# Performance work log

Hardware: AMD Instinct MI355X
Metric: run time of the kernel (lower is better)

The kernel has to match this reference:

```python
import jax, jax.numpy as jnp
import numpy as np


def setup_inputs() -> dict:
    key = jax.random.key(0)
    embeddings = jax.random.normal(key, (4, 2048, 128), dtype=jnp.float32)
    return {"embeddings": embeddings}


def _pairwise_dist(x):
    # x: [N, D] -> Euclidean distance matrix [N, N] (matches torch.cdist, p=2)
    sq = jnp.sum(x * x, axis=-1)  # [N]
    d2 = sq[:, None] + sq[None, :] - 2.0 * (x @ x.T)
    d2 = jnp.maximum(d2, 0.0)
    # safe sqrt: exact 0 on the diagonal / coincident points, no NaN grads
    safe = jnp.where(d2 > 0.0, d2, 1.0)
    return jnp.where(d2 > 0.0, jnp.sqrt(safe), 0.0)


def reference(embeddings) -> jnp.ndarray:
    b, s, d = embeddings.shape
    x = embeddings.reshape(b * s, d)
    dist = _pairwise_dist(x)                 # [N, N]
    mean_dist = jnp.mean(dist)
    # torch.std default: unbiased (ddof=1) over all elements
    std_dist = jnp.std(dist, ddof=1)
    return std_dist / (mean_dist + 1e-08)
```

## Files before the change

kernel.cpp:

```cpp
#include <hip/hip_runtime.h>
#include <hip/hip_bf16.h>
#include <math.h>


#define NPTS   8192
#define DIM    128
#define TILE   128
#define KHALF  64
#define NTILES (NPTS / TILE)
#define NTOT   (NTILES * (NTILES + 1) / 2)

typedef __attribute__((ext_vector_type(8))) short short8;
typedef __attribute__((ext_vector_type(4))) float f32x4;

typedef const __attribute__((address_space(1))) void* gas_ptr;
typedef __attribute__((address_space(3))) void* las_ptr;

__device__ __forceinline__ void gload16(const void* g, void* l) {
    __builtin_amdgcn_global_load_lds((gas_ptr)g, (las_ptr)l, 16, 0, 0);
}

__global__ __launch_bounds__(256)
void ph_prep(const float* __restrict__ x, ushort* __restrict__ xb,
             float* __restrict__ sq)
{
    const int tid = threadIdx.x;
    const int row = blockIdx.x * 32 + (tid >> 3);
    const int seg = tid & 7;
    const float4* p = reinterpret_cast<const float4*>(x + (size_t)row * DIM + seg * 16);
    float v[16];
    {
        float4 a = p[0], b = p[1], c = p[2], d = p[3];
        v[0]=a.x; v[1]=a.y; v[2]=a.z; v[3]=a.w;  v[4]=b.x; v[5]=b.y; v[6]=b.z; v[7]=b.w;
        v[8]=c.x; v[9]=c.y; v[10]=c.z; v[11]=c.w; v[12]=d.x; v[13]=d.y; v[14]=d.z; v[15]=d.w;
    }
    float s = 0.f;
    ushort h[16];
#pragma unroll
    for (int j = 0; j < 16; ++j) {
        __hip_bfloat16 hb = __float2bfloat16(v[j]);
        h[j] = *reinterpret_cast<ushort*>(&hb);
        s = fmaf(v[j], v[j], s);
    }
    short8 o0, o1;
#pragma unroll
    for (int j = 0; j < 8; ++j) { o0[j] = (short)h[j]; o1[j] = (short)h[j+8]; }
    short8* dst = reinterpret_cast<short8*>(xb + (size_t)row * DIM + seg * 16);
    dst[0] = o0; dst[1] = o1;
    s += __shfl_xor(s, 1); s += __shfl_xor(s, 2); s += __shfl_xor(s, 4);
    if (seg == 0) sq[row] = s;
}

__global__ __launch_bounds__(256)
void ph_gram(const ushort* __restrict__ xb, const float* __restrict__ sq,
             double* __restrict__ partials)
{
    const int f   = blockIdx.x;
    const int tid = threadIdx.x;

    int bi = (int)((129.0f - sqrtf((float)(16641 - 8 * f))) * 0.5f);
    while ((bi + 1) * 64 - ((bi + 1) * bi) / 2 <= f) ++bi;
    while (bi * 64 - (bi * (bi - 1)) / 2 > f) --bi;
    const int bj = bi + (f - (bi * 64 - (bi * (bi - 1)) / 2));

    __shared__ ushort As[TILE * KHALF];
    __shared__ ushort Bs[TILE * KHALF];
    __shared__ float  nA[TILE], nB[TILE];
    __shared__ double rr[8];

    const int lane = tid & 63;
    const int wv   = tid >> 6;
    const int wr   = wv >> 1, wc = wv & 1;

    if (tid < 128) nA[tid]       = sq[bi * TILE + tid];
    else           nB[tid - 128] = sq[bj * TILE + (tid - 128)];

    const char* gA = (const char*)(xb + (size_t)bi * TILE * DIM);
    const char* gB = (const char*)(xb + (size_t)bj * TILE * DIM);

    const int srow = lane >> 3;
    const int skb  = (lane & 7) * 16;
#define STAGE(h)                                                              \
    {                                                                         \
        _Pragma("unroll")                                                     \
        for (int c = 0; c < 4; ++c) {                                         \
            const int chunk = wv * 4 + c;                                     \
            const int row   = chunk * 8 + srow;                               \
            const int gkb   = (h) * 128 + (skb ^ ((row & 7) << 4));           \
            const size_t go = (size_t)row * 256 + gkb;                        \
            gload16(gA + go, (char*)As + chunk * 1024);                       \
            gload16(gB + go, (char*)Bs + chunk * 1024);                       \
        }                                                                     \
    }

    f32x4 acc[4][4];
#pragma unroll
    for (int m = 0; m < 4; ++m)
#pragma unroll
        for (int n = 0; n < 4; ++n) acc[m][n] = (f32x4){0.f, 0.f, 0.f, 0.f};

    STAGE(0);
    __syncthreads();

#pragma unroll
    for (int h = 0; h < 2; ++h) {
#pragma unroll
        for (int kk = 0; kk < 2; ++kk) {
            const int kb = kk * 64 + (lane >> 4) * 16;
            short8 af[4], bfr[4];
#pragma unroll
            for (int m = 0; m < 4; ++m) {
                const int row = wr * 64 + m * 16 + (lane & 15);
                af[m] = *reinterpret_cast<const short8*>(
                    (const char*)As + row * 128 + (kb ^ ((row & 7) << 4)));
            }
#pragma unroll
            for (int n = 0; n < 4; ++n) {
                const int col = wc * 64 + n * 16 + (lane & 15);
                bfr[n] = *reinterpret_cast<const short8*>(
                    (const char*)Bs + col * 128 + (kb ^ ((col & 7) << 4)));
            }
#pragma unroll
            for (int m = 0; m < 4; ++m)
#pragma unroll
                for (int n = 0; n < 4; ++n)
                    acc[m][n] = __builtin_amdgcn_mfma_f32_16x16x32_bf16(
                        af[m], bfr[n], acc[m][n], 0, 0, 0);
        }
        if (h == 0) {
            __syncthreads();
            STAGE(1);
            __syncthreads();
        }
    }

    float s1 = 0.f, s2 = 0.f;
    const bool diag = (bi == bj);
#pragma unroll
    for (int m = 0; m < 4; ++m) {
        float nAr[4];
#pragma unroll
        for (int r = 0; r < 4; ++r) nAr[r] = nA[wr*64 + m*16 + (lane>>4)*4 + r];
#pragma unroll
        for (int n = 0; n < 4; ++n) {
            const int col  = wc*64 + n*16 + (lane & 15);
            const float nBc = nB[col];
#pragma unroll
            for (int r = 0; r < 4; ++r) {
                float d2 = fmaf(-2.f, acc[m][n][r], nAr[r] + nBc);
                d2 = fmaxf(d2, 0.f);
                if (diag) {
                    const int row = wr*64 + m*16 + (lane>>4)*4 + r;
                    if (row == col) d2 = 0.f;
                }
                s1 += sqrtf(d2);
                s2 += d2;
            }
        }
    }
#pragma unroll
    for (int off = 1; off < 64; off <<= 1) {
        s1 += __shfl_xor(s1, off);
        s2 += __shfl_xor(s2, off);
    }
    const double w = diag ? 1.0 : 2.0;
    if (lane == 0) { rr[wv] = (double)s1 * w; rr[4 + wv] = (double)s2 * w; }
    __syncthreads();
    if (tid == 0) {
        partials[2*f]     = rr[0] + rr[1] + rr[2] + rr[3];
        partials[2*f + 1] = rr[4] + rr[5] + rr[6] + rr[7];
    }
#undef STAGE
}

__global__ __launch_bounds__(256)
void ph_finalize(const double* __restrict__ partials, float* __restrict__ out)
{
    __shared__ double r1[256], r2[256];
    const int tid = threadIdx.x;
    double s1 = 0.0, s2 = 0.0;
    for (int i = tid; i < NTOT; i += 256) { s1 += partials[2*i]; s2 += partials[2*i+1]; }
    r1[tid] = s1; r2[tid] = s2;
    __syncthreads();
    for (int off = 128; off > 0; off >>= 1) {
        if (tid < off) { r1[tid] += r1[tid+off]; r2[tid] += r2[tid+off]; }
        __syncthreads();
    }
    if (tid == 0) {
        const double M    = (double)NPTS * (double)NPTS;
        const double mean = r1[0] / M;
        double var = (r2[0] - r1[0]*r1[0]/M) / (M - 1.0);
        if (var < 0.0) var = 0.0;
        out[0] = (float)(sqrt(var) / (mean + 1e-8));
    }
}

#define LSTR 132
__global__ __launch_bounds__(256)
void ph_pair_kernel(const float* __restrict__ x, double* __restrict__ partials)
{
    const int bi  = blockIdx.y;
    const int bj  = blockIdx.x;
    const int tid = threadIdx.x;
    const int flat = bi * NTILES + bj;
    if (bj < bi) {
        if (tid == 0) { partials[2*flat] = 0.0; partials[2*flat+1] = 0.0; }
        return;
    }
    __shared__ __align__(16) float As[TILE * LSTR];
    __shared__ __align__(16) float Bs[TILE * LSTR];
    __shared__ float  nA[TILE];
    __shared__ float  nB[TILE];
    __shared__ double red1[256];
    __shared__ double red2[256];
    const float* Ab = x + (size_t)bi * TILE * DIM;
    const float* Bb = x + (size_t)bj * TILE * DIM;
#pragma unroll
    for (int it = 0; it < 16; ++it) {
        const int e   = (tid + it * 256) * 4;
        const int row = e >> 7;
        const int k   = e & 127;
        float4 va = *reinterpret_cast<const float4*>(Ab + e);
        As[(k+0)*LSTR + row] = va.x; As[(k+1)*LSTR + row] = va.y;
        As[(k+2)*LSTR + row] = va.z; As[(k+3)*LSTR + row] = va.w;
        float4 vb = *reinterpret_cast<const float4*>(Bb + e);
        Bs[(k+0)*LSTR + row] = vb.x; Bs[(k+1)*LSTR + row] = vb.y;
        Bs[(k+2)*LSTR + row] = vb.z; Bs[(k+3)*LSTR + row] = vb.w;
    }
    __syncthreads();
    if (tid < 128) {
        float s = 0.f;
#pragma unroll 8
        for (int k = 0; k < DIM; ++k) { float v = As[k*LSTR + tid]; s = fmaf(v, v, s); }
        nA[tid] = s;
    } else {
        const int r = tid - 128;
        float s = 0.f;
#pragma unroll 8
        for (int k = 0; k < DIM; ++k) { float v = Bs[k*LSTR + r]; s = fmaf(v, v, s); }
        nB[r] = s;
    }
    __syncthreads();
    const int tx = tid & 15, ty = tid >> 4;
    const int ra = ty * 8, cb = tx * 8;
    float acc[8][8];
#pragma unroll
    for (int r = 0; r < 8; ++r)
#pragma unroll
        for (int c = 0; c < 8; ++c) acc[r][c] = 0.f;
#pragma unroll 4
    for (int k = 0; k < DIM; ++k) {
        const float4 a0 = *reinterpret_cast<const float4*>(&As[k*LSTR + ra]);
        const float4 a1 = *reinterpret_cast<const float4*>(&As[k*LSTR + ra + 4]);
        const float4 b0 = *reinterpret_cast<const float4*>(&Bs[k*LSTR + cb]);
        const float4 b1 = *reinterpret_cast<const float4*>(&Bs[k*LSTR + cb + 4]);
        const float a[8] = {a0.x,a0.y,a0.z,a0.w,a1.x,a1.y,a1.z,a1.w};
        const float b[8] = {b0.x,b0.y,b0.z,b0.w,b1.x,b1.y,b1.z,b1.w};
#pragma unroll
        for (int r = 0; r < 8; ++r)
#pragma unroll
            for (int c = 0; c < 8; ++c)
                acc[r][c] = fmaf(a[r], b[c], acc[r][c]);
    }
    double s1 = 0.0, s2 = 0.0;
    const int gi0 = bi*TILE + ra, gj0 = bj*TILE + cb;
#pragma unroll
    for (int r = 0; r < 8; ++r) {
#pragma unroll
        for (int c = 0; c < 8; ++c) {
            float d2 = nA[ra+r] + nB[cb+c] - 2.0f * acc[r][c];
            d2 = fmaxf(d2, 0.0f);
            if (gi0 + r == gj0 + c) d2 = 0.0f;
            s1 += (double)sqrtf(d2);
            s2 += (double)d2;
        }
    }
    const double w = (bi == bj) ? 1.0 : 2.0;
    s1 *= w; s2 *= w;
    red1[tid] = s1; red2[tid] = s2;
    __syncthreads();
    for (int off = 128; off > 0; off >>= 1) {
        if (tid < off) { red1[tid] += red1[tid+off]; red2[tid] += red2[tid+off]; }
        __syncthreads();
    }
    if (tid == 0) { partials[2*flat] = red1[0]; partials[2*flat+1] = red2[0]; }
}

__global__ __launch_bounds__(256)
void ph_finalize_sq(const double* __restrict__ partials, float* __restrict__ out)
{
    __shared__ double r1[256], r2[256];
    const int tid = threadIdx.x;
    double s1 = 0.0, s2 = 0.0;
    for (int i = tid; i < NTILES*NTILES; i += 256) { s1 += partials[2*i]; s2 += partials[2*i+1]; }
    r1[tid] = s1; r2[tid] = s2;
    __syncthreads();
    for (int off = 128; off > 0; off >>= 1) {
        if (tid < off) { r1[tid] += r1[tid+off]; r2[tid] += r2[tid+off]; }
        __syncthreads();
    }
    if (tid == 0) {
        const double M    = (double)NPTS * (double)NPTS;
        const double mean = r1[0] / M;
        double var = (r2[0] - r1[0]*r1[0]/M) / (M - 1.0);
        if (var < 0.0) var = 0.0;
        out[0] = (float)(sqrt(var) / (mean + 1e-8));
    }
}

extern "C" void kernel_launch(void* const* d_in, const int* in_sizes, int n_in,
                              void* d_out, int out_size, void* d_ws, size_t ws_size,
                              hipStream_t stream)
{
    const float* x = (const float*)d_in[0];
    float* out     = (float*)d_out;

    const size_t XB_OFF = 0;
    const size_t SQ_OFF = (size_t)NPTS * DIM * sizeof(ushort);
    const size_t PT_OFF = SQ_OFF + NPTS * sizeof(float);
    const size_t NEEDED = PT_OFF + (size_t)NTOT * 2 * sizeof(double);

    if (ws_size >= NEEDED) {
        ushort* xb       = (ushort*)((char*)d_ws + XB_OFF);
        float*  sq       = (float*) ((char*)d_ws + SQ_OFF);
        double* partials = (double*)((char*)d_ws + PT_OFF);

        ph_prep<<<NPTS / 32, 256, 0, stream>>>(x, xb, sq);
        ph_gram<<<NTOT, 256, 0, stream>>>(xb, sq, partials);
        ph_finalize<<<1, 256, 0, stream>>>(partials, out);
    } else {
        double* partials = (double*)d_ws;
        ph_pair_kernel<<<dim3(NTILES, NTILES), 256, 0, stream>>>(x, partials);
        ph_finalize_sq<<<1, 256, 0, stream>>>(partials, out);
    }
}
```

Measured before the change: 41.82 us.

## Load MFMA operands directly from global memory, dropping LDS staging

The gram kernel no longer stages A/B tiles through LDS with global_load_lds and barriers. Each lane now loads its bf16 MFMA fragments straight from global (L2-resident) memory, and reads the squared norms from global too. Launch bounds now request 3 blocks per CU. This removes the LDS traffic and the mid-loop syncs, but each wave reloads data its neighbours share, which raises global/L2 traffic and exposes load latency.

```diff
diff --git a/kernel.cpp b/kernel.cpp
--- a/kernel.cpp
+++ b/kernel.cpp
@@ -6,19 +6,11 @@
 #define NPTS   8192
 #define DIM    128
 #define TILE   128
-#define KHALF  64
 #define NTILES (NPTS / TILE)
 #define NTOT   (NTILES * (NTILES + 1) / 2)
 
 typedef __attribute__((ext_vector_type(8))) short short8;
 typedef __attribute__((ext_vector_type(4))) float f32x4;
-
-typedef const __attribute__((address_space(1))) void* gas_ptr;
-typedef __attribute__((address_space(3))) void* las_ptr;
-
-__device__ __forceinline__ void gload16(const void* g, void* l) {
-    __builtin_amdgcn_global_load_lds((gas_ptr)g, (las_ptr)l, 16, 0, 0);
-}
 
 __global__ __launch_bounds__(256)
 void ph_prep(const float* __restrict__ x, ushort* __restrict__ xb,
@@ -51,7 +43,7 @@
     if (seg == 0) sq[row] = s;
 }
 
-__global__ __launch_bounds__(256)
+__global__ __launch_bounds__(256, 3)
 void ph_gram(const ushort* __restrict__ xb, const float* __restrict__ sq,
              double* __restrict__ partials)
 {
@@ -63,35 +55,20 @@
     while (bi * 64 - (bi * (bi - 1)) / 2 > f) --bi;
     const int bj = bi + (f - (bi * 64 - (bi * (bi - 1)) / 2));
 
-    __shared__ ushort As[TILE * KHALF];
-    __shared__ ushort Bs[TILE * KHALF];
-    __shared__ float  nA[TILE], nB[TILE];
-    __shared__ double rr[8];
-
     const int lane = tid & 63;
     const int wv   = tid >> 6;
     const int wr   = wv >> 1, wc = wv & 1;
 
-    if (tid < 128) nA[tid]       = sq[bi * TILE + tid];
-    else           nB[tid - 128] = sq[bj * TILE + (tid - 128)];
-
-    const char* gA = (const char*)(xb + (size_t)bi * TILE * DIM);
-    const char* gB = (const char*)(xb + (size_t)bj * TILE * DIM);
-
-    const int srow = lane >> 3;
-    const int skb  = (lane & 7) * 16;
-#define STAGE(h)                                                              \
-    {                                                                         \
-        _Pragma("unroll")                                                     \
-        for (int c = 0; c < 4; ++c) {                                         \
-            const int chunk = wv * 4 + c;                                     \
-            const int row   = chunk * 8 + srow;                               \
-            const int gkb   = (h) * 128 + (skb ^ ((row & 7) << 4));           \
-            const size_t go = (size_t)row * 256 + gkb;                        \
-            gload16(gA + go, (char*)As + chunk * 1024);                       \
-            gload16(gB + go, (char*)Bs + chunk * 1024);                       \
-        }                                                                     \
-    }
+    const char* base = (const char*)xb;
+    const int   koff = (lane >> 4) * 16;
+    const char* pA[4];
+    const char* pB[4];
+#pragma unroll
+    for (int m = 0; m < 4; ++m)
+        pA[m] = base + (size_t)(bi*TILE + wr*64 + m*16 + (lane & 15)) * 256 + koff;
+#pragma unroll
+    for (int n = 0; n < 4; ++n)
+        pB[n] = base + (size_t)(bj*TILE + wc*64 + n*16 + (lane & 15)) * 256 + koff;
 
     f32x4 acc[4][4];
 #pragma unroll
@@ -99,52 +76,36 @@
 #pragma unroll
         for (int n = 0; n < 4; ++n) acc[m][n] = (f32x4){0.f, 0.f, 0.f, 0.f};
 
-    STAGE(0);
-    __syncthreads();
-
-#pragma unroll
-    for (int h = 0; h < 2; ++h) {
-#pragma unroll
-        for (int kk = 0; kk < 2; ++kk) {
-            const int kb = kk * 64 + (lane >> 4) * 16;
-            short8 af[4], bfr[4];
-#pragma unroll
-            for (int m = 0; m < 4; ++m) {
-                const int row = wr * 64 + m * 16 + (lane & 15);
-                af[m] = *reinterpret_cast<const short8*>(
-                    (const char*)As + row * 128 + (kb ^ ((row & 7) << 4)));
-            }
-#pragma unroll
-            for (int n = 0; n < 4; ++n) {
-                const int col = wc * 64 + n * 16 + (lane & 15);
-                bfr[n] = *reinterpret_cast<const short8*>(
-                    (const char*)Bs + col * 128 + (kb ^ ((col & 7) << 4)));
-            }
-#pragma unroll
-            for (int m = 0; m < 4; ++m)
-#pragma unroll
-                for (int n = 0; n < 4; ++n)
-                    acc[m][n] = __builtin_amdgcn_mfma_f32_16x16x32_bf16(
-                        af[m], bfr[n], acc[m][n], 0, 0, 0);
-        }
-        if (h == 0) {
-            __syncthreads();
-            STAGE(1);
-            __syncthreads();
-        }
-    }
-
+#pragma unroll
+    for (int kk = 0; kk < 4; ++kk) {
+        short8 af[4], bfr[4];
+#pragma unroll
+        for (int m = 0; m < 4; ++m)
+            af[m]  = *reinterpret_cast<const short8*>(pA[m] + kk * 64);
+#pragma unroll
+        for (int n = 0; n < 4; ++n)
+            bfr[n] = *reinterpret_cast<const short8*>(pB[n] + kk * 64);
+#pragma unroll
+        for (int m = 0; m < 4; ++m)
+#pragma unroll
+            for (int n = 0; n < 4; ++n)
+                acc[m][n] = __builtin_amdgcn_mfma_f32_16x16x32_bf16(
+                    af[m], bfr[n], acc[m][n], 0, 0, 0);
+    }
+
+    const float* sqA = sq + bi * TILE;
+    const float* sqB = sq + bj * TILE;
     float s1 = 0.f, s2 = 0.f;
     const bool diag = (bi == bj);
 #pragma unroll
     for (int m = 0; m < 4; ++m) {
         float nAr[4];
 #pragma unroll
-        for (int r = 0; r < 4; ++r) nAr[r] = nA[wr*64 + m*16 + (lane>>4)*4 + r];
+        for (int r = 0; r < 4; ++r) nAr[r] = sqA[wr*64 + m*16 + (lane>>4)*4 + r];
 #pragma unroll
         for (int n = 0; n < 4; ++n) {
-            const int col  = wc*64 + n*16 + (lane & 15);
-            const float nBc = nB[col];
+            const int col   = wc*64 + n*16 + (lane & 15);
+            const float nBc = sqB[col];
 #pragma unroll
             for (int r = 0; r < 4; ++r) {
                 float d2 = fmaf(-2.f, acc[m][n][r], nAr[r] + nBc);
@@ -163,6 +124,8 @@
         s1 += __shfl_xor(s1, off);
         s2 += __shfl_xor(s2, off);
     }
+
+    __shared__ double rr[8];
     const double w = diag ? 1.0 : 2.0;
     if (lane == 0) { rr[wv] = (double)s1 * w; rr[4 + wv] = (double)s2 * w; }
     __syncthreads();
@@ -170,7 +133,6 @@
         partials[2*f]     = rr[0] + rr[1] + rr[2] + rr[3];
         partials[2*f + 1] = rr[4] + rr[5] + rr[6] + rr[7];
     }
-#undef STAGE
 }
 
 __global__ __launch_bounds__(256)
```

Result: slower. 59.74 us (+42.9%).

## Load full K tiles into LDS in one stage and read norms from registers

Applied to the files above, without the earlier changes.

The Gram kernel now stages the whole 128-wide K dimension of both tiles into shared memory in one pass, instead of two halves separated by barriers. Removing the mid-loop sync-restage-sync sequence lets all global loads be in flight together. The squared norms are loaded straight from global memory into registers rather than going through shared memory. The epilogue is split into diagonal and off-diagonal paths with two accumulators each for more ILP. Shared memory per block doubles to 64 KB, which may limit how many blocks fit on each CU.

```diff
diff --git a/kernel.cpp b/kernel.cpp
--- a/kernel.cpp
+++ b/kernel.cpp
@@ -6,7 +6,6 @@
 #define NPTS   8192
 #define DIM    128
 #define TILE   128
-#define KHALF  64
 #define NTILES (NPTS / TILE)
 #define NTOT   (NTILES * (NTILES + 1) / 2)
 
@@ -63,35 +62,37 @@
     while (bi * 64 - (bi * (bi - 1)) / 2 > f) --bi;
     const int bj = bi + (f - (bi * 64 - (bi * (bi - 1)) / 2));
 
-    __shared__ ushort As[TILE * KHALF];
-    __shared__ ushort Bs[TILE * KHALF];
-    __shared__ float  nA[TILE], nB[TILE];
+    __shared__ ushort As[TILE * DIM];
+    __shared__ ushort Bs[TILE * DIM];
     __shared__ double rr[8];
 
     const int lane = tid & 63;
     const int wv   = tid >> 6;
     const int wr   = wv >> 1, wc = wv & 1;
 
-    if (tid < 128) nA[tid]       = sq[bi * TILE + tid];
-    else           nB[tid - 128] = sq[bj * TILE + (tid - 128)];
-
     const char* gA = (const char*)(xb + (size_t)bi * TILE * DIM);
     const char* gB = (const char*)(xb + (size_t)bj * TILE * DIM);
 
-    const int srow = lane >> 3;
-    const int skb  = (lane & 7) * 16;
-#define STAGE(h)                                                              \
-    {                                                                         \
-        _Pragma("unroll")                                                     \
-        for (int c = 0; c < 4; ++c) {                                         \
-            const int chunk = wv * 4 + c;                                     \
-            const int row   = chunk * 8 + srow;                               \
-            const int gkb   = (h) * 128 + (skb ^ ((row & 7) << 4));           \
-            const size_t go = (size_t)row * 256 + gkb;                        \
-            gload16(gA + go, (char*)As + chunk * 1024);                       \
-            gload16(gB + go, (char*)Bs + chunk * 1024);                       \
-        }                                                                     \
-    }
+    const int srow = lane >> 4;
+    const int skb  = (lane & 15) * 16;
+#pragma unroll
+    for (int c = 0; c < 8; ++c) {
+        const int chunk = wv * 8 + c;
+        const int row   = chunk * 4 + srow;
+        const int kbl   = skb ^ ((row & 7) << 4);
+        const size_t go = (size_t)row * 256 + kbl;
+        gload16(gA + go, (char*)As + chunk * 1024);
+        gload16(gB + go, (char*)Bs + chunk * 1024);
+    }
+
+    const float* sqA = sq + bi * TILE + wr * 64 + (lane >> 4) * 4;
+    const float* sqB = sq + bj * TILE + wc * 64 + (lane & 15);
+    float4 nAr[4];
+    float  nBc[4];
+#pragma unroll
+    for (int m = 0; m < 4; ++m) nAr[m] = *reinterpret_cast<const float4*>(sqA + m * 16);
+#pragma unroll
+    for (int n = 0; n < 4; ++n) nBc[n] = sqB[n * 16];
 
     f32x4 acc[4][4];
 #pragma unroll
@@ -99,65 +100,71 @@
 #pragma unroll
         for (int n = 0; n < 4; ++n) acc[m][n] = (f32x4){0.f, 0.f, 0.f, 0.f};
 
-    STAGE(0);
-    __syncthreads();
-
-#pragma unroll
-    for (int h = 0; h < 2; ++h) {
-#pragma unroll
-        for (int kk = 0; kk < 2; ++kk) {
-            const int kb = kk * 64 + (lane >> 4) * 16;
-            short8 af[4], bfr[4];
-#pragma unroll
-            for (int m = 0; m < 4; ++m) {
-                const int row = wr * 64 + m * 16 + (lane & 15);
-                af[m] = *reinterpret_cast<const short8*>(
-                    (const char*)As + row * 128 + (kb ^ ((row & 7) << 4)));
+    __syncthreads();
+
+#pragma unroll
+    for (int kk = 0; kk < 4; ++kk) {
+        const int kb = kk * 64 + (lane >> 4) * 16;
+        short8 af[4], bfr[4];
+#pragma unroll
+        for (int m = 0; m < 4; ++m) {
+            const int row = wr * 64 + m * 16 + (lane & 15);
+            af[m] = *reinterpret_cast<const short8*>(
+                (const char*)As + row * 256 + (kb ^ ((row & 7) << 4)));
+        }
+#pragma unroll
+        for (int n = 0; n < 4; ++n) {
+            const int col = wc * 64 + n * 16 + (lane & 15);
+            bfr[n] = *reinterpret_cast<const short8*>(
+                (const char*)Bs + col * 256 + (kb ^ ((col & 7) << 4)));
+        }
+#pragma unroll
+        for (int m = 0; m < 4; ++m)
+#pragma unroll
+            for (int n = 0; n < 4; ++n)
+                acc[m][n] = __builtin_amdgcn_mfma_f32_16x16x32_bf16(
+                    af[m], bfr[n], acc[m][n], 0, 0, 0);
+    }
+
+    float s1a = 0.f, s1b = 0.f, s2a = 0.f, s2b = 0.f;
+    const bool diag = (bi == bj);
+    if (!diag) {
+#pragma unroll
+        for (int m = 0; m < 4; ++m) {
+#pragma unroll
+            for (int n = 0; n < 4; ++n) {
+                const float pre0 = nAr[m].x + nBc[n];
+                const float pre1 = nAr[m].y + nBc[n];
+                const float pre2 = nAr[m].z + nBc[n];
+                const float pre3 = nAr[m].w + nBc[n];
+                float d0 = fmaxf(fmaf(-2.f, acc[m][n][0], pre0), 0.f);
+                float d1 = fmaxf(fmaf(-2.f, acc[m][n][1], pre1), 0.f);
+                float d2 = fmaxf(fmaf(-2.f, acc[m][n][2], pre2), 0.f);
+                float d3 = fmaxf(fmaf(-2.f, acc[m][n][3], pre3), 0.f);
+                s1a += sqrtf(d0); s1b += sqrtf(d1);
+                s1a += sqrtf(d2); s1b += sqrtf(d3);
+                s2a += d0 + d2;   s2b += d1 + d3;
             }
+        }
+    } else {
+#pragma unroll
+        for (int m = 0; m < 4; ++m) {
 #pragma unroll
             for (int n = 0; n < 4; ++n) {
-                const int col = wc * 64 + n * 16 + (lane & 15);
-                bfr[n] = *reinterpret_cast<const short8*>(
-                    (const char*)Bs + col * 128 + (kb ^ ((col & 7) << 4)));
+#pragma unroll
+                for (int r = 0; r < 4; ++r) {
+                    const int row = wr*64 + m*16 + (lane>>4)*4 + r;
+                    const int col = wc*64 + n*16 + (lane & 15);
+                    const float nA_ = (r==0)?nAr[m].x:(r==1)?nAr[m].y:(r==2)?nAr[m].z:nAr[m].w;
+                    float d2 = fmaxf(fmaf(-2.f, acc[m][n][r], nA_ + nBc[n]), 0.f);
+                    if (row == col) d2 = 0.f;
+                    s1a += sqrtf(d2);
+                    s2a += d2;
+                }
             }
-#pragma unroll
-            for (int m = 0; m < 4; ++m)
-#pragma unroll
-                for (int n = 0; n < 4; ++n)
-                    acc[m][n] = __builtin_amdgcn_mfma_f32_16x16x32_bf16(
-                        af[m], bfr[n], acc[m][n], 0, 0, 0);
-        }
-        if (h == 0) {
-            __syncthreads();
-            STAGE(1);
-            __syncthreads();
-        }
-    }
-
-    float s1 = 0.f, s2 = 0.f;
-    const bool diag = (bi == bj);
-#pragma unroll
-    for (int m = 0; m < 4; ++m) {
-        float nAr[4];
-#pragma unroll
-        for (int r = 0; r < 4; ++r) nAr[r] = nA[wr*64 + m*16 + (lane>>4)*4 + r];
-#pragma unroll
-        for (int n = 0; n < 4; ++n) {
-            const int col  = wc*64 + n*16 + (lane & 15);
-            const float nBc = nB[col];
-#pragma unroll
-            for (int r = 0; r < 4; ++r) {
-                float d2 = fmaf(-2.f, acc[m][n][r], nAr[r] + nBc);
-                d2 = fmaxf(d2, 0.f);
-                if (diag) {
-                    const int row = wr*64 + m*16 + (lane>>4)*4 + r;
-                    if (row == col) d2 = 0.f;
-                }
-                s1 += sqrtf(d2);
-                s2 += d2;
-            }
-        }
-    }
+        }
+    }
+    float s1 = (s1a + s1b), s2 = (s2a + s2b);
 #pragma unroll
     for (int off = 1; off < 64; off <<= 1) {
         s1 += __shfl_xor(s1, off);
@@ -170,7 +177,6 @@
         partials[2*f]     = rr[0] + rr[1] + rr[2] + rr[3];
         partials[2*f + 1] = rr[4] + rr[5] + rr[6] + rr[7];
     }
-#undef STAGE
 }
 
 __global__ __launch_bounds__(256)
```

After: 44.11 us. +5.5%, slower.

## Enlarge gram tiles to 256x256 with 512 threads and double-buffered K staging

Applied to the files above, without the earlier changes.

The gram kernel now processes 256x256 output tiles with 8 waves, each holding an 8x4 MFMA accumulator block. The two K halves are staged into separate LDS buffers, so the second half's load overlaps the first half's compute and one barrier is dropped. The epilogue reads norms directly from global memory, uses a hardware sqrt builtin, and splits accumulators to break dependency chains. The changes aim to raise reuse and cut per-block overhead, but there are now only 528 blocks on a 256-CU part, which increases tail imbalance, and LDS and register use per block go up.

```diff
diff --git a/kernel.cpp b/kernel.cpp
--- a/kernel.cpp
+++ b/kernel.cpp
@@ -5,10 +5,11 @@
 
 #define NPTS   8192
 #define DIM    128
-#define TILE   128
-#define KHALF  64
-#define NTILES (NPTS / TILE)
-#define NTOT   (NTILES * (NTILES + 1) / 2)
+#define BT     256
+#define NT2    (NPTS / BT)
+#define NBLK   (NT2 * (NT2 + 1) / 2)
+#define NTILES (NPTS / 128)
+#define NTOTSQ (NTILES * NTILES)
 
 typedef __attribute__((ext_vector_type(8))) short short8;
 typedef __attribute__((ext_vector_type(4))) float f32x4;
@@ -18,6 +19,10 @@
 
 __device__ __forceinline__ void gload16(const void* g, void* l) {
     __builtin_amdgcn_global_load_lds((gas_ptr)g, (las_ptr)l, 16, 0, 0);
+}
+
+__device__ __forceinline__ float fsqrt(float x) {
+    return __builtin_amdgcn_sqrtf(x);
 }
 
 __global__ __launch_bounds__(256)
@@ -51,126 +56,148 @@
     if (seg == 0) sq[row] = s;
 }
 
-__global__ __launch_bounds__(256)
+__global__ __launch_bounds__(512)
 void ph_gram(const ushort* __restrict__ xb, const float* __restrict__ sq,
              double* __restrict__ partials)
 {
     const int f   = blockIdx.x;
     const int tid = threadIdx.x;
 
-    int bi = (int)((129.0f - sqrtf((float)(16641 - 8 * f))) * 0.5f);
-    while ((bi + 1) * 64 - ((bi + 1) * bi) / 2 <= f) ++bi;
-    while (bi * 64 - (bi * (bi - 1)) / 2 > f) --bi;
-    const int bj = bi + (f - (bi * 64 - (bi * (bi - 1)) / 2));
-
-    __shared__ ushort As[TILE * KHALF];
-    __shared__ ushort Bs[TILE * KHALF];
-    __shared__ float  nA[TILE], nB[TILE];
-    __shared__ double rr[8];
+    int bi = (int)((65.0f - fsqrt((float)(4225 - 8 * f))) * 0.5f);
+    while ((bi + 1) * 32 - ((bi + 1) * bi) / 2 <= f) ++bi;
+    while (bi * 32 - (bi * (bi - 1)) / 2 > f) --bi;
+    const int bj = bi + (f - (bi * 32 - (bi * (bi - 1)) / 2));
+
+    __shared__ ushort A0[BT * 64], B0[BT * 64];
+    __shared__ ushort A1[BT * 64], B1[BT * 64];
+    __shared__ double rr[16];
 
     const int lane = tid & 63;
     const int wv   = tid >> 6;
-    const int wr   = wv >> 1, wc = wv & 1;
-
-    if (tid < 128) nA[tid]       = sq[bi * TILE + tid];
-    else           nB[tid - 128] = sq[bj * TILE + (tid - 128)];
-
-    const char* gA = (const char*)(xb + (size_t)bi * TILE * DIM);
-    const char* gB = (const char*)(xb + (size_t)bj * TILE * DIM);
-
-    const int srow = lane >> 3;
-    const int skb  = (lane & 7) * 16;
-#define STAGE(h)                                                              \
+    const int wr2  = wv >> 2;
+    const int wc4  = wv & 3;
+
+    const char* gA = (const char*)(xb + (size_t)bi * BT * DIM);
+    const char* gB = (const char*)(xb + (size_t)bj * BT * DIM);
+
+    const bool  stA  = wv < 4;
+    const char* gsrc = stA ? gA : gB;
+    const int   cb0  = (wv & 3) * 8;
+    const int   srow = lane >> 3;
+    const int   skb  = (lane & 7) * 16;
+
+#define STAGE(h, dA, dB)                                                      \
+    {                                                                         \
+        char* dst_ = stA ? (char*)(dA) : (char*)(dB);                         \
+        _Pragma("unroll")                                                     \
+        for (int c = 0; c < 8; ++c) {                                         \
+            const int chunk = cb0 + c;                                        \
+            const int row   = chunk * 8 + srow;                               \
+            const size_t go = (size_t)row * 256 + (h) * 128                   \
+                              + (skb ^ ((row & 7) << 4));                     \
+            gload16(gsrc + go, dst_ + chunk * 1024);                          \
+        }                                                                     \
+    }
+
+    f32x4 acc[8][4];
+#pragma unroll
+    for (int m = 0; m < 8; ++m)
+#pragma unroll
+        for (int n = 0; n < 4; ++n) acc[m][n] = (f32x4){0.f, 0.f, 0.f, 0.f};
+
+#define COMPUTE(dA, dB)                                                       \
     {                                                                         \
         _Pragma("unroll")                                                     \
-        for (int c = 0; c < 4; ++c) {                                         \
-            const int chunk = wv * 4 + c;                                     \
-            const int row   = chunk * 8 + srow;                               \
-            const int gkb   = (h) * 128 + (skb ^ ((row & 7) << 4));           \
-            const size_t go = (size_t)row * 256 + gkb;                        \
-            gload16(gA + go, (char*)As + chunk * 1024);                       \
-            gload16(gB + go, (char*)Bs + chunk * 1024);                       \
+        for (int ks = 0; ks < 2; ++ks) {                                      \
+            const int kb = ks * 64 + (lane >> 4) * 16;                        \
+            short8 af[8], bfr[4];                                             \
+            _Pragma("unroll")                                                 \
+            for (int m = 0; m < 8; ++m) {                                     \
+                const int row = wr2 * 128 + m * 16 + (lane & 15);             \
+                af[m] = *reinterpret_cast<const short8*>(                     \
+                    (const char*)(dA) + row * 128 + (kb ^ ((row & 7) << 4))); \
+            }                                                                 \
+            _Pragma("unroll")                                                 \
+            for (int n = 0; n < 4; ++n) {                                     \
+                const int col = wc4 * 64 + n * 16 + (lane & 15);              \
+                bfr[n] = *reinterpret_cast<const short8*>(                    \
+                    (const char*)(dB) + col * 128 + (kb ^ ((col & 7) << 4))); \
+            }                                                                 \
+            _Pragma("unroll")                                                 \
+            for (int m = 0; m < 8; ++m)                                       \
+                _Pragma("unroll")                                             \
+                for (int n = 0; n < 4; ++n)                                   \
+                    acc[m][n] = __builtin_amdgcn_mfma_f32_16x16x32_bf16(      \
+                        af[m], bfr[n], acc[m][n], 0, 0, 0);                   \
         }                                                                     \
     }
 
-    f32x4 acc[4][4];
-#pragma unroll
-    for (int m = 0; m < 4; ++m)
-#pragma unroll
-        for (int n = 0; n < 4; ++n) acc[m][n] = (f32x4){0.f, 0.f, 0.f, 0.f};
-
-    STAGE(0);
-    __syncthreads();
-
-#pragma unroll
-    for (int h = 0; h < 2; ++h) {
-#pragma unroll
-        for (int kk = 0; kk < 2; ++kk) {
-            const int kb = kk * 64 + (lane >> 4) * 16;
-            short8 af[4], bfr[4];
-#pragma unroll
-            for (int m = 0; m < 4; ++m) {
-                const int row = wr * 64 + m * 16 + (lane & 15);
-                af[m] = *reinterpret_cast<const short8*>(
-                    (const char*)As + row * 128 + (kb ^ ((row & 7) << 4)));
-            }
+    STAGE(0, A0, B0);
+    __syncthreads();
+    STAGE(1, A1, B1);
+    COMPUTE(A0, B0);
+    __syncthreads();
+    COMPUTE(A1, B1);
+
+    const float* sqA = sq + bi * BT + wr2 * 128 + (lane >> 4) * 4;
+    const float* sqB = sq + bj * BT + wc4 * 64 + (lane & 15);
+    float nB_[4];
+#pragma unroll
+    for (int n = 0; n < 4; ++n) nB_[n] = sqB[n * 16];
+
+    float s1a = 0.f, s1b = 0.f, s2a = 0.f, s2b = 0.f;
+    const bool diag = (bi == bj);
+    if (!diag) {
+#pragma unroll
+        for (int m = 0; m < 8; ++m) {
+            const float4 na = *reinterpret_cast<const float4*>(sqA + m * 16);
 #pragma unroll
             for (int n = 0; n < 4; ++n) {
-                const int col = wc * 64 + n * 16 + (lane & 15);
-                bfr[n] = *reinterpret_cast<const short8*>(
-                    (const char*)Bs + col * 128 + (kb ^ ((col & 7) << 4)));
-            }
-#pragma unroll
-            for (int m = 0; m < 4; ++m)
-#pragma unroll
-                for (int n = 0; n < 4; ++n)
-                    acc[m][n] = __builtin_amdgcn_mfma_f32_16x16x32_bf16(
-                        af[m], bfr[n], acc[m][n], 0, 0, 0);
-        }
-        if (h == 0) {
-            __syncthreads();
-            STAGE(1);
-            __syncthreads();
-        }
-    }
-
-    float s1 = 0.f, s2 = 0.f;
-    const bool diag = (bi == bj);
-#pragma unroll
-    for (int m = 0; m < 4; ++m) {
-        float nAr[4];
-#pragma unroll
-        for (int r = 0; r < 4; ++r) nAr[r] = nA[wr*64 + m*16 + (lane>>4)*4 + r];
-#pragma unroll
-        for (int n = 0; n < 4; ++n) {
-            const int col  = wc*64 + n*16 + (lane & 15);
-            const float nBc = nB[col];
-#pragma unroll
-            for (int r = 0; r < 4; ++r) {
-                float d2 = fmaf(-2.f, acc[m][n][r], nAr[r] + nBc);
-                d2 = fmaxf(d2, 0.f);
-                if (diag) {
-                    const int row = wr*64 + m*16 + (lane>>4)*4 + r;
-                    if (row == col) d2 = 0.f;
-                }
-                s1 += sqrtf(d2);
-                s2 += d2;
+                float d0 = fmaxf(fmaf(-2.f, acc[m][n][0], na.x + nB_[n]), 0.f);
+                float d1 = fmaxf(fmaf(-2.f, acc[m][n][1], na.y + nB_[n]), 0.f);
+                float d2 = fmaxf(fmaf(-2.f, acc[m][n][2], na.z + nB_[n]), 0.f);
+                float d3 = fmaxf(fmaf(-2.f, acc[m][n][3], na.w + nB_[n]), 0.f);
+                s1a += fsqrt(d0); s1b += fsqrt(d1);
+                s1a += fsqrt(d2); s1b += fsqrt(d3);
+                s2a += d0 + d2;   s2b += d1 + d3;
             }
         }
-    }
+    } else {
+#pragma unroll
+        for (int m = 0; m < 8; ++m) {
+            const float4 na = *reinterpret_cast<const float4*>(sqA + m * 16);
+            const float nav[4] = {na.x, na.y, na.z, na.w};
+#pragma unroll
+            for (int n = 0; n < 4; ++n) {
+                const int col = wc4 * 64 + n * 16 + (lane & 15);
+#pragma unroll
+                for (int r = 0; r < 4; ++r) {
+                    const int row = wr2 * 128 + m * 16 + (lane >> 4) * 4 + r;
+                    float d = fmaxf(fmaf(-2.f, acc[m][n][r], nav[r] + nB_[n]), 0.f);
+                    if (row == col) d = 0.f;
+                    s1a += fsqrt(d);
+                    s2a += d;
+                }
+            }
+        }
+    }
+    float s1 = s1a + s1b, s2 = s2a + s2b;
 #pragma unroll
     for (int off = 1; off < 64; off <<= 1) {
         s1 += __shfl_xor(s1, off);
         s2 += __shfl_xor(s2, off);
     }
     const double w = diag ? 1.0 : 2.0;
-    if (lane == 0) { rr[wv] = (double)s1 * w; rr[4 + wv] = (double)s2 * w; }
+    if (lane == 0) { rr[wv] = (double)s1 * w; rr[8 + wv] = (double)s2 * w; }
     __syncthreads();
     if (tid == 0) {
-        partials[2*f]     = rr[0] + rr[1] + rr[2] + rr[3];
-        partials[2*f + 1] = rr[4] + rr[5] + rr[6] + rr[7];
+        double t1 = 0.0, t2 = 0.0;
+#pragma unroll
+        for (int i = 0; i < 8; ++i) { t1 += rr[i]; t2 += rr[8 + i]; }
+        partials[2*f] = t1; partials[2*f + 1] = t2;
     }
 #undef STAGE
+#undef COMPUTE
 }
 
 __global__ __launch_bounds__(256)
@@ -179,7 +206,7 @@
     __shared__ double r1[256], r2[256];
     const int tid = threadIdx.x;
     double s1 = 0.0, s2 = 0.0;
-    for (int i = tid; i < NTOT; i += 256) { s1 += partials[2*i]; s2 += partials[2*i+1]; }
+    for (int i = tid; i < NBLK; i += 256) { s1 += partials[2*i]; s2 += partials[2*i+1]; }
     r1[tid] = s1; r2[tid] = s2;
     __syncthreads();
     for (int off = 128; off > 0; off >>= 1) {
@@ -207,14 +234,14 @@
         if (tid == 0) { partials[2*flat] = 0.0; partials[2*flat+1] = 0.0; }
         return;
     }
-    __shared__ __align__(16) float As[TILE * LSTR];
-    __shared__ __align__(16) float Bs[TILE * LSTR];
-    __shared__ float  nA[TILE];
-    __shared__ float  nB[TILE];
+    __shared__ __align__(16) float As[128 * LSTR];
+    __shared__ __align__(16) float Bs[128 * LSTR];
+    __shared__ float  nA[128];
+    __shared__ float  nB[128];
     __shared__ double red1[256];
     __shared__ double red2[256];
-    const float* Ab = x + (size_t)bi * TILE * DIM;
-    const float* Bb = x + (size_t)bj * TILE * DIM;
+    const float* Ab = x + (size_t)bi * 128 * DIM;
+    const float* Bb = x + (size_t)bj * 128 * DIM;
 #pragma unroll
     for (int it = 0; it < 16; ++it) {
         const int e   = (tid + it * 256) * 4;
@@ -263,7 +290,7 @@
                 acc[r][c] = fmaf(a[r], b[c], acc[r][c]);
     }
     double s1 = 0.0, s2 = 0.0;
-    const int gi0 = bi*TILE + ra, gj0 = bj*TILE + cb;
+    const int gi0 = bi*128 + ra, gj0 = bj*128 + cb;
 #pragma unroll
     for (int r = 0; r < 8; ++r) {
 #pragma unroll
@@ -292,7 +319,7 @@
     __shared__ double r1[256], r2[256];
     const int tid = threadIdx.x;
     double s1 = 0.0, s2 = 0.0;
-    for (int i = tid; i < NTILES*NTILES; i += 256) { s1 += partials[2*i]; s2 += partials[2*i+1]; }
+    for (int i = tid; i < NTOTSQ; i += 256) { s1 += partials[2*i]; s2 += partials[2*i+1]; }
     r1[tid] = s1; r2[tid] = s2;
     __syncthreads();
     for (int off = 128; off > 0; off >>= 1) {
@@ -318,7 +345,7 @@
     const size_t XB_OFF = 0;
     const size_t SQ_OFF = (size_t)NPTS * DIM * sizeof(ushort);
     const size_t PT_OFF = SQ_OFF + NPTS * sizeof(float);
-    const size_t NEEDED = PT_OFF + (size_t)NTOT * 2 * sizeof(double);
+    const size_t NEEDED = PT_OFF + (size_t)NTOTSQ * 2 * sizeof(double);
 
     if (ws_size >= NEEDED) {
         ushort* xb       = (ushort*)((char*)d_ws + XB_OFF);
@@ -326,7 +353,7 @@
         double* partials = (double*)((char*)d_ws + PT_OFF);
 
         ph_prep<<<NPTS / 32, 256, 0, stream>>>(x, xb, sq);
-        ph_gram<<<NTOT, 256, 0, stream>>>(xb, sq, partials);
+        ph_gram<<<NBLK, 512, 0, stream>>>(xb, sq, partials);
         ph_finalize<<<1, 256, 0, stream>>>(partials, out);
     } else {
         double* partials = (double*)d_ws;
```

After: 33.75 us. 19.3% less time.
